# Kernel tuning notes

Hardware: AMD Instinct MI355X
Metric: run time of the kernel (lower is better)

## Reference

```python
import jax, jax.numpy as jnp
import numpy as np
from jax import lax

BN_EPS = 1e-5


def conv(x, w, b, pad):
    # x: NCHW, w: OIHW
    y = lax.conv_general_dilated(x, w, (1, 1), [(pad, pad), (pad, pad)],
                                 dimension_numbers=('NCHW', 'OIHW', 'NCHW'))
    return y + b[None, :, None, None]


def conv_t(x, w, b):
    # ConvTranspose2d, stride=1, padding=0, kernel 3. w is torch layout [in, out, kh, kw].
    # Equivalent to a regular conv with spatially flipped kernel, in/out swapped, full padding (kh-1=2).
    wf = jnp.transpose(jnp.flip(w, (2, 3)), (1, 0, 2, 3))  # [out, in, kh, kw]
    y = lax.conv_general_dilated(x, wf, (1, 1), [(2, 2), (2, 2)],
                                 dimension_numbers=('NCHW', 'OIHW', 'NCHW'))
    return y + b[None, :, None, None]


def bn(x, g, be):
    # BatchNorm2d, training-mode batch stats (biased variance), gamma/beta learnable.
    mu = x.mean((0, 2, 3), keepdims=True)
    var = x.var((0, 2, 3), keepdims=True)
    xn = (x - mu) * lax.rsqrt(var + BN_EPS)
    return g[None, :, None, None] * xn + be[None, :, None, None]


def setup_inputs() -> dict:
    key = jax.random.key(0)
    ks = jax.random.split(key, 20)
    B, C, H, W = 16, 64, 44, 44
    P = H * W  # 1936

    def kaiming(k, shape, fan_out):
        return jax.random.normal(k, shape, jnp.float32) * np.sqrt(2.0 / fan_out)

    inp = {
        'depth': jax.random.normal(ks[0], (B, C, H, W), jnp.float32),
        'rgb': jax.random.normal(ks[1], (B, C, H, W), jnp.float32),
        # h_c / h_f conv layers: Conv2d(128, 64, 3, padding=1)
        'w_hc': kaiming(ks[2], (64, 128, 3, 3), 64 * 9), 'b_hc': jnp.zeros((64,), jnp.float32),
        'w_hf': kaiming(ks[3], (64, 128, 3, 3), 64 * 9), 'b_hf': jnp.zeros((64,), jnp.float32),
        # spatial_pool_agr
        'w_s1': kaiming(ks[4], (32, P, 3, 3), 32 * 9), 'bs1': jnp.zeros((32,), jnp.float32),
        'g1': jnp.ones((32,), jnp.float32), 'be1': jnp.zeros((32,), jnp.float32),
        'w_s2': kaiming(ks[5], (32, 32, 3, 3), 32 * 9), 'bs2': jnp.zeros((32,), jnp.float32),
        'g2': jnp.ones((32,), jnp.float32), 'be2': jnp.zeros((32,), jnp.float32),
        # ConvTranspose2d weights in torch layout [in, out, kh, kw]
        'w_d1': kaiming(ks[6], (32, 32, 3, 3), 32 * 9), 'bd1': jnp.zeros((32,), jnp.float32),
        'g3': jnp.ones((32,), jnp.float32), 'be3': jnp.zeros((32,), jnp.float32),
        'w_d2': kaiming(ks[7], (32, 1, 3, 3), 1 * 9), 'bd2': jnp.zeros((1,), jnp.float32),
        # channel_pool_ag: Linear(64, 16), Linear(16, 64)
        'w_l1': kaiming(ks[8], (16, 64), 16), 'bl1': jnp.zeros((16,), jnp.float32),
        'w_l2': kaiming(ks[9], (64, 16), 64), 'bl2': jnp.zeros((64,), jnp.float32),
    }
    return inp


def reference(depth, rgb, w_hc, b_hc, w_hf, b_hf,
              w_s1, bs1, g1, be1, w_s2, bs2, g2, be2,
              w_d1, bd1, g3, be3, w_d2, bd2,
              w_l1, bl1, w_l2, bl2):
    B, C, H, W = depth.shape
    # fused rgb+depth conv
    h_c = jnp.concatenate([rgb, depth], axis=1)          # [B, 2C, H, W]
    h_c_conv = jax.nn.relu(conv(h_c, w_hc, b_hc, 1))      # [B, 64, H, W]

    # per-pixel correlation: grouped 1x1 conv == batched matmul
    # pixel_corr[b, p, y, x] = sum_c rgb[b, c, y, x] * depth[b, c, p]
    pixel_corr = jnp.einsum('bchw,bcp->bphw', rgb, depth.reshape(B, C, H * W))

    x = jax.nn.relu(bn(conv(pixel_corr, w_s1, bs1, 0), g1, be1))  # 44 -> 42
    x = jax.nn.relu(bn(conv(x, w_s2, bs2, 0), g2, be2))           # 42 -> 40
    x = jax.nn.relu(bn(conv_t(x, w_d1, bd1), g3, be3))            # 40 -> 42
    spatial_att = jax.nn.sigmoid(conv_t(x, w_d2, bd2))            # [B, 1, 44, 44]

    # per-channel correlation: grouped full-extent conv == elementwise dot per (b, c)
    depth_corr = jnp.sum(rgb * depth, axis=(2, 3))                # [B, C]
    # MaxPool2d(1)/AvgPool2d(1) are identities -> both branches are identical
    def mlp(v):
        return jax.nn.relu(v @ w_l1.T + bl1) @ w_l2.T + bl2
    m = mlp(depth_corr)
    channel_att = jax.nn.sigmoid(m + m)[:, :, None, None]         # [B, C, 1, 1]

    h_att = jnp.concatenate([h_c_conv * spatial_att, h_c_conv * channel_att], axis=1)
    return jax.nn.relu(conv(h_att, w_hf, b_hf, 1))                # [B, 64, 44, 44]
```

## Files before the change

kernel.cpp:

```cpp
#include <hip/hip_runtime.h>
#include <math.h>

#define P_ 1936
#define EPS_ 1e-5f

typedef __attribute__((ext_vector_type(8))) short bf16x8;
typedef __attribute__((ext_vector_type(4))) float f32x4;
typedef __attribute__((ext_vector_type(4))) ushort u16x4;

__device__ __forceinline__ ushort f2bf(float f) {
    union { float f; unsigned u; } v; v.f = f;
    unsigned u = v.u;
    return (ushort)((u + 0x7FFFu + ((u >> 16) & 1u)) >> 16);
}
__device__ __forceinline__ float bf2f(ushort h) {
    union { unsigned u; float f; } v; v.u = (unsigned)h << 16;
    return v.f;
}

__device__ __forceinline__ void bn_coef(const float* stats, const float* g,
                                        const float* be, int ch, float inv_n,
                                        float& sc, float& sh) {
    float sum = stats[ch*2], sq = stats[ch*2+1];
    float mu = sum * inv_n;
    float var = sq * inv_n - mu*mu;
    float r = rsqrtf(var + EPS_);
    sc = g[ch] * r;
    sh = be[ch] - mu * sc;
}

__global__ __launch_bounds__(256) void k_setup(const float* __restrict__ whc,
                                               const float* __restrict__ whf,
                                               const float* __restrict__ ws2,
                                               const float* __restrict__ wd1,
                                               const float* __restrict__ ws1,
                                               const float* __restrict__ rgb,
                                               const float* __restrict__ depth,
                                               ushort* __restrict__ wpck,
                                               ushort* __restrict__ a2,
                                               ushort* __restrict__ a3,
                                               ushort* __restrict__ apck1,
                                               ushort* __restrict__ xp,
                                               ushort* __restrict__ depthb,
                                               float* __restrict__ dcor_part,
                                               float* __restrict__ stats) {
    __shared__ float r8[8];
    const int bx = blockIdx.x, t = threadIdx.x;
    if (bx < 2808) {
        if (bx == 0 && t < 192) stats[t] = 0.f;
        int idx = bx * 256 + t;
        if (idx < 147456) {
            const float* src = (idx < 73728) ? whc : whf;
            int j = (idx < 73728) ? idx : idx - 73728;
            int kk = j / 8192, rem = j - kk * 8192;
            int o = rem >> 7, c = rem & 127;
            wpck[(idx < 73728 ? 0 : 73728) + (kk * 64 + o) * 128 + c] =
                f2bf(src[(size_t)(o * 128 + c) * 9 + kk]);
        } else if (idx < 156672) {
            int j = idx - 147456;
            int kk = j >> 10, rem = j & 1023, o = rem >> 5, c = rem & 31;
            a2[j] = f2bf(ws2[((size_t)o*32 + c)*9 + kk]);
            a3[j] = f2bf(wd1[((size_t)c*32 + o)*9 + (8 - kk)]);
        } else if (idx < 718848) {
            int j = idx - 156672;
            int m = j / 1952, p = j - m*1952;
            int o = m / 9, kk = m - o*9;
            apck1[j] = (p < P_) ? f2bf(ws1[((size_t)o*P_ + p)*9 + kk]) : (ushort)0;
        }
        return;
    }
    const int j = bx - 2808;
    const int g8 = j & 7, b = (j >> 3) & 15, q = j >> 7;
    const int c0 = g8 * 8;
    const float* rsrc = rgb   + ((size_t)b*64 + c0)*P_;
    const float* dsrc = depth + ((size_t)b*64 + c0)*P_;
    ushort* xr = xp + ((size_t)(b*16 + g8))*2300*8;
    ushort* xd = xp + ((size_t)(b*16 + 8 + g8))*2300*8;
    if (t < 8) r8[t] = 0.f;
    __syncthreads();
    float dc[8];
    #pragma unroll
    for (int e = 0; e < 8; ++e) dc[e] = 0.f;

    const int pbase = q * 575;
    for (int pos = pbase + t; pos < pbase + 575; pos += 256) {
        int y1 = pos / 50, x1 = pos - y1*50;
        uint4 vr = {0u,0u,0u,0u}, vd = {0u,0u,0u,0u};
        if (y1 >= 1 && y1 <= 44 && x1 >= 1 && x1 <= 44) {
            int p = (y1-1)*44 + (x1-1);
            ushort hr[8], hd[8];
            #pragma unroll
            for (int e = 0; e < 8; ++e) {
                float fr = rsrc[(size_t)e*P_ + p];
                float fd = dsrc[(size_t)e*P_ + p];
                dc[e] = fmaf(fr, fd, dc[e]);
                hr[e] = f2bf(fr); hd[e] = f2bf(fd);
            }
            vr.x = hr[0] | ((unsigned)hr[1] << 16); vr.y = hr[2] | ((unsigned)hr[3] << 16);
            vr.z = hr[4] | ((unsigned)hr[5] << 16); vr.w = hr[6] | ((unsigned)hr[7] << 16);
            vd.x = hd[0] | ((unsigned)hd[1] << 16); vd.y = hd[2] | ((unsigned)hd[3] << 16);
            vd.z = hd[4] | ((unsigned)hd[5] << 16); vd.w = hd[6] | ((unsigned)hd[7] << 16);
        }
        *(uint4*)(xr + (size_t)pos*8) = vr;
        *(uint4*)(xd + (size_t)pos*8) = vd;
    }
    for (int idx = q*976 + t; idx < q*976 + 976; idx += 256) {
        int e = idx / 488, jj = idx - e*488;
        u16x4 h = {0,0,0,0};
        if (jj < 484) {
            float4 f4 = *(const float4*)(dsrc + (size_t)e*P_ + jj*4);
            h[0] = f2bf(f4.x); h[1] = f2bf(f4.y); h[2] = f2bf(f4.z); h[3] = f2bf(f4.w);
        }
        *(u16x4*)(depthb + ((size_t)(b*64 + c0 + e))*1952 + jj*4) = h;
    }
    #pragma unroll
    for (int e = 0; e < 8; ++e) {
        float v = dc[e];
        #pragma unroll
        for (int off = 32; off > 0; off >>= 1) v += __shfl_down(v, off, 64);
        if ((t & 63) == 0) atomicAdd(&r8[e], v);
    }
    __syncthreads();
    if (t < 8) dcor_part[q*1024 + b*64 + c0 + t] = r8[t];
}

__global__ __launch_bounds__(256) void k_front(const ushort* __restrict__ xp,
                                               const ushort* __restrict__ wt,
                                               const float* __restrict__ bhc,
                                               ushort* __restrict__ hcp,
                                               const ushort* __restrict__ apck1,
                                               const ushort* __restrict__ depthb,
                                               ushort* __restrict__ upck,
                                               const float* __restrict__ dcor_part,
                                               const float* __restrict__ wl1,
                                               const float* __restrict__ bl1,
                                               const float* __restrict__ wl2,
                                               const float* __restrict__ bl2,
                                               float* __restrict__ catt) {
    __shared__ ushort lds[9616];
    __shared__ float mlpb[80];
    const int bx = blockIdx.x, t = threadIdx.x;
    if (bx < 352) {
        const int rt = bx % 11, og = (bx / 11) & 1, b = bx / 22;
        const int w = t >> 6, lane = t & 63, lr = lane & 15, lg = lane >> 4;
        const int r0 = rt * 4;
        f32x4 acc[2][3];
        #pragma unroll
        for (int mf = 0; mf < 2; ++mf)
            #pragma unroll
            for (int nf = 0; nf < 3; ++nf)
                acc[mf][nf] = (f32x4){0.f, 0.f, 0.f, 0.f};

        for (int s = 0; s < 4; ++s) {
            __syncthreads();
            const ushort* gsrc = xp + ((size_t)(b*16 + s*4))*2300*8;
            for (int u = t; u < 1200; u += 256) {
                int cg = u / 300, rem = u - cg*300;
                int rr = rem / 50, xx = rem - rr*50;
                uint4 v = *(const uint4*)(gsrc + (((size_t)cg*46 + (r0+rr))*50 + xx)*8);
                *(uint4*)(lds + (size_t)u*8) = v;
            }
            __syncthreads();
            const int abase = s*32 + lg*8;
            #pragma unroll
            for (int kk = 0; kk < 9; ++kk) {
                bf16x8 af[2];
                #pragma unroll
                for (int mf = 0; mf < 2; ++mf)
                    af[mf] = *(const bf16x8*)(wt + (size_t)(kk*64 + og*32 + mf*16 + lr)*128 + abase);
                const int ky = kk / 3, kx = kk - ky*3;
                #pragma unroll
                for (int nf = 0; nf < 3; ++nf) {
                    bf16x8 bf = *(const bf16x8*)&lds[((lg*6 + (w + ky))*50 + (nf*16 + lr + kx))*8];
                    #pragma unroll
                    for (int mf = 0; mf < 2; ++mf)
                        acc[mf][nf] = __builtin_amdgcn_mfma_f32_16x16x32_bf16(af[mf], bf, acc[mf][nf], 0, 0, 0);
                }
            }
        }
        const int y = r0 + w;
        #pragma unroll
        for (int nf = 0; nf < 3; ++nf) {
            int x = nf*16 + lr;
            if (x < 44) {
                #pragma unroll
                for (int mf = 0; mf < 2; ++mf) {
                    u16x4 pk;
                    #pragma unroll
                    for (int i = 0; i < 4; ++i) {
                        int ol = og*32 + mf*16 + lg*4 + i;
                        pk[i] = f2bf(fmaxf(acc[mf][nf][i] + bhc[ol], 0.f));
                    }
                    int g = og*4 + mf*2 + (lg >> 1);
                    *(u16x4*)(hcp + (((size_t)(b*8 + g)*46 + (y+1))*50 + (x+1))*8 + (lg&1)*4) = pk;
                }
            }
        }
        return;
    }
    const int j = bx - 352;
    const int mt = j % 19, b = j / 19;
    if (mt == 18) {
        float* dcs = mlpb;
        float* h   = mlpb + 64;
        if (t < 64) dcs[t] = dcor_part[b*64 + t] + dcor_part[1024 + b*64 + t]
                           + dcor_part[2048 + b*64 + t] + dcor_part[3072 + b*64 + t];
        __syncthreads();
        if (t < 16) {
            float a = bl1[t];
            #pragma unroll 8
            for (int c = 0; c < 64; ++c) a = fmaf(dcs[c], wl1[t*64 + c], a);
            h[t] = fmaxf(a, 0.f);
        }
        __syncthreads();
        if (t < 64) {
            float m = bl2[t];
            #pragma unroll
            for (int jj = 0; jj < 16; ++jj) m = fmaf(h[jj], wl2[t*16 + jj], m);
            catt[b*64 + t] = 1.f / (1.f + expf(-2.f*m));
        }
        return;
    }
    const int nt = t >> 6, lane = t & 63, lr = lane & 15, lg = lane >> 4;
    f32x4 acc = (f32x4){0.f, 0.f, 0.f, 0.f};
    const ushort* ap = apck1 + (size_t)(mt*16 + lr)*1952 + lg*8;
    const ushort* bp = depthb + ((size_t)(b*64) + nt*16 + lr)*1952 + lg*8;
    #pragma unroll 4
    for (int ks = 0; ks < 61; ++ks) {
        bf16x8 af = *(const bf16x8*)(ap + ks*32);
        bf16x8 bf = *(const bf16x8*)(bp + ks*32);
        acc = __builtin_amdgcn_mfma_f32_16x16x32_bf16(af, bf, acc, 0, 0, 0);
    }
    #pragma unroll
    for (int i = 0; i < 4; ++i) {
        int m = mt*16 + lg*4 + i;
        int o = m / 9, kk = m - o*9;
        upck[((size_t)(b*9 + kk)*32 + o)*64 + nt*16 + lr] = f2bf(acc[i]);
    }
}

__global__ __launch_bounds__(256) void k_conv1_mfma(const ushort* __restrict__ xp,
                                                    const ushort* __restrict__ upck,
                                                    const float* __restrict__ bs1,
                                                    ushort* __restrict__ z1p,
                                                    float* __restrict__ stats) {
    __shared__ ushort lds[8*6*50*8 + 32];
    __shared__ float ssum[32], ssq[32];
    const int rt = blockIdx.x, b = blockIdx.y, t = threadIdx.x;
    const int w = t >> 6, lane = t & 63, lr = lane & 15, lg = lane >> 4;
    const int r0 = rt * 4;
    if (t < 32) { ssum[t] = 0.f; ssq[t] = 0.f; }
    f32x4 acc[2][3];
    #pragma unroll
    for (int mf = 0; mf < 2; ++mf)
        #pragma unroll
        for (int nf = 0; nf < 3; ++nf)
            acc[mf][nf] = (f32x4){0.f, 0.f, 0.f, 0.f};

    const ushort* gsrc = xp + (size_t)b*16*2300*8;
    for (int u = t; u < 2400; u += 256) {
        int cg = u / 300, rem = u - cg*300;
        int rr = rem / 50, xx = rem - rr*50;
        int y1 = min(r0 + 1 + rr, 45);
        *(uint4*)(lds + (size_t)u*8) = *(const uint4*)(gsrc + (((size_t)cg*46 + y1)*50 + xx)*8);
    }
    __syncthreads();
    #pragma unroll
    for (int s = 0; s < 2; ++s) {
        #pragma unroll
        for (int kk = 0; kk < 9; ++kk) {
            bf16x8 af[2];
            #pragma unroll
            for (int mf = 0; mf < 2; ++mf)
                af[mf] = *(const bf16x8*)(upck + ((size_t)(b*9 + kk)*32 + mf*16 + lr)*64 + s*32 + lg*8);
            const int ky = kk / 3, kx = kk - ky*3;
            #pragma unroll
            for (int nf = 0; nf < 3; ++nf) {
                bf16x8 bv = *(const bf16x8*)&lds[(((s*4 + lg)*6 + (w + ky))*50 + (nf*16 + lr + kx + 1))*8];
                #pragma unroll
                for (int mf = 0; mf < 2; ++mf)
                    acc[mf][nf] = __builtin_amdgcn_mfma_f32_16x16x32_bf16(af[mf], bv, acc[mf][nf], 0, 0, 0);
            }
        }
    }
    const int y = r0 + w;
    const int cb = lg*4;
    if (y < 42) {
        float ls[2][4], lq[2][4], br[2][4];
        #pragma unroll
        for (int mf = 0; mf < 2; ++mf)
            #pragma unroll
            for (int i = 0; i < 4; ++i) {
                ls[mf][i] = 0.f; lq[mf][i] = 0.f;
                br[mf][i] = bs1[mf*16 + cb + i];
            }
        #pragma unroll
        for (int nf = 0; nf < 3; ++nf) {
            int x = nf*16 + lr;
            bool xv = (x < 42);
            #pragma unroll
            for (int mf = 0; mf < 2; ++mf) {
                u16x4 pk;
                #pragma unroll
                for (int i = 0; i < 4; ++i) {
                    float v = acc[mf][nf][i] + br[mf][i];
                    if (xv) { ls[mf][i] += v; lq[mf][i] = fmaf(v, v, lq[mf][i]); }
                    pk[i] = f2bf(v);
                }
                if (xv) {
                    int cg1 = mf*2 + (lg >> 1);
                    *(u16x4*)(z1p + ((((size_t)b*4 + cg1)*42 + y)*48 + x)*8 + (lg&1)*4) = pk;
                }
            }
        }
        #pragma unroll
        for (int mf = 0; mf < 2; ++mf)
            #pragma unroll
            for (int i = 0; i < 4; ++i) {
                float s0 = ls[mf][i], q0 = lq[mf][i];
                #pragma unroll
                for (int m = 1; m < 16; m <<= 1) { s0 += __shfl_xor(s0, m, 64); q0 += __shfl_xor(q0, m, 64); }
                if (lr == 0) { atomicAdd(&ssum[mf*16 + cb + i], s0); atomicAdd(&ssq[mf*16 + cb + i], q0); }
            }
    }
    __syncthreads();
    if (t < 32) { atomicAdd(&stats[t*2], ssum[t]); atomicAdd(&stats[t*2+1], ssq[t]); }
}

__global__ __launch_bounds__(256) void k_conv2_mfma(const ushort* __restrict__ z1p,
                                                    const ushort* __restrict__ apck,
                                                    const float* __restrict__ bs2,
                                                    const float* __restrict__ g1,
                                                    const float* __restrict__ be1,
                                                    const float* __restrict__ statsIn,
                                                    ushort* __restrict__ z2p,
                                                    float* __restrict__ statsOut) {
    __shared__ ushort lds[4*6*48*8 + 32];
    __shared__ float sc[32], sh[32], ssum[32], ssq[32];
    const int rt = blockIdx.x, b = blockIdx.y, t = threadIdx.x;
    const int w = t >> 6, lane = t & 63, lr = lane & 15, lg = lane >> 4;
    const int r0 = rt * 4;
    if (t < 32) {
        bn_coef(statsIn, g1, be1, t, 1.f/28224.f, sc[t], sh[t]);
        ssum[t] = 0.f; ssq[t] = 0.f;
    }
    __syncthreads();
    f32x4 acc[2][3];
    #pragma unroll
    for (int mf = 0; mf < 2; ++mf)
        #pragma unroll
        for (int nf = 0; nf < 3; ++nf)
            acc[mf][nf] = (f32x4){0.f, 0.f, 0.f, 0.f};

    for (int u = t; u < 1152; u += 256) {
        int cg = u / 288, rem = u - cg*288;
        int rr = rem / 48, xx = rem - rr*48;
        uint4 raw = *(const uint4*)(z1p + ((((size_t)b*4 + cg)*42 + (r0 + rr))*48 + xx)*8);
        unsigned arr[4] = {raw.x, raw.y, raw.z, raw.w};
        ushort h[8];
        #pragma unroll
        for (int e = 0; e < 8; ++e) {
            ushort hv = (e & 1) ? (ushort)(arr[e>>1] >> 16) : (ushort)(arr[e>>1] & 0xffffu);
            float f = fmaxf(fmaf(bf2f(hv), sc[cg*8 + e], sh[cg*8 + e]), 0.f);
            h[e] = f2bf(f);
        }
        uint4 v;
        v.x = h[0] | ((unsigned)h[1] << 16);
        v.y = h[2] | ((unsigned)h[3] << 16);
        v.z = h[4] | ((unsigned)h[5] << 16);
        v.w = h[6] | ((unsigned)h[7] << 16);
        *(uint4*)(lds + (size_t)u*8) = v;
    }
    __syncthreads();
    #pragma unroll
    for (int kk = 0; kk < 9; ++kk) {
        bf16x8 af[2];
        #pragma unroll
        for (int mf = 0; mf < 2; ++mf)
            af[mf] = *(const bf16x8*)(apck + (size_t)(kk*32 + mf*16 + lr)*32 + lg*8);
        const int ky = kk / 3, kx = kk - ky*3;
        #pragma unroll
        for (int nf = 0; nf < 3; ++nf) {
            bf16x8 bv = *(const bf16x8*)&lds[((lg*6 + (w + ky))*48 + (nf*16 + lr + kx))*8];
            #pragma unroll
            for (int mf = 0; mf < 2; ++mf)
                acc[mf][nf] = __builtin_amdgcn_mfma_f32_16x16x32_bf16(af[mf], bv, acc[mf][nf], 0, 0, 0);
        }
    }
    const int y = r0 + w;
    const int cb = lg*4;
    {
        float ls[2][4], lq[2][4], br[2][4];
        #pragma unroll
        for (int mf = 0; mf < 2; ++mf)
            #pragma unroll
            for (int i = 0; i < 4; ++i) {
                ls[mf][i] = 0.f; lq[mf][i] = 0.f;
                br[mf][i] = bs2[mf*16 + cb + i];
            }
        #pragma unroll
        for (int nf = 0; nf < 3; ++nf) {
            int x = nf*16 + lr;
            bool xv = (x < 40);
            #pragma unroll
            for (int mf = 0; mf < 2; ++mf) {
                u16x4 pk;
                #pragma unroll
                for (int i = 0; i < 4; ++i) {
                    float v = acc[mf][nf][i] + br[mf][i];
                    if (xv) { ls[mf][i] += v; lq[mf][i] = fmaf(v, v, lq[mf][i]); }
                    pk[i] = f2bf(v);
                }
                if (xv) {
                    int cg1 = mf*2 + (lg >> 1);
                    *(u16x4*)(z2p + ((((size_t)b*4 + cg1)*46 + (y+2))*48 + (x+2))*8 + (lg&1)*4) = pk;
                }
            }
        }
        #pragma unroll
        for (int mf = 0; mf < 2; ++mf)
            #pragma unroll
            for (int i = 0; i < 4; ++i) {
                float s0 = ls[mf][i], q0 = lq[mf][i];
                #pragma unroll
                for (int m = 1; m < 16; m <<= 1) { s0 += __shfl_xor(s0, m, 64); q0 += __shfl_xor(q0, m, 64); }
                if (lr == 0) { atomicAdd(&ssum[mf*16 + cb + i], s0); atomicAdd(&ssq[mf*16 + cb + i], q0); }
            }
    }
    __syncthreads();
    if (t < 32) { atomicAdd(&statsOut[t*2], ssum[t]); atomicAdd(&statsOut[t*2+1], ssq[t]); }
}

__global__ __launch_bounds__(256) void k_dconv1_mfma(const ushort* __restrict__ z2p,
                                                     const ushort* __restrict__ apck,
                                                     const float* __restrict__ bd1,
                                                     const float* __restrict__ g2,
                                                     const float* __restrict__ be2,
                                                     const float* __restrict__ statsIn,
                                                     ushort* __restrict__ z3p,
                                                     float* __restrict__ statsOut) {
    __shared__ ushort lds[4*6*48*8 + 32];
    __shared__ float sc[32], sh[32], ssum[32], ssq[32];
    const int rt = blockIdx.x, b = blockIdx.y, t = threadIdx.x;
    const int w = t >> 6, lane = t & 63, lr = lane & 15, lg = lane >> 4;
    const int r0 = rt * 4;
    if (t < 32) {
        bn_coef(statsIn, g2, be2, t, 1.f/25600.f, sc[t], sh[t]);
        ssum[t] = 0.f; ssq[t] = 0.f;
    }
    __syncthreads();
    f32x4 acc[2][3];
    #pragma unroll
    for (int mf = 0; mf < 2; ++mf)
        #pragma unroll
        for (int nf = 0; nf < 3; ++nf)
            acc[mf][nf] = (f32x4){0.f, 0.f, 0.f, 0.f};

    for (int u = t; u < 1152; u += 256) {
        int cg = u / 288, rem = u - cg*288;
        int rr = rem / 48, xx = rem - rr*48;
        int row = r0 + rr;
        uint4 v = {0u,0u,0u,0u};
        if (row >= 2 && row <= 41 && xx >= 2 && xx <= 41) {
            uint4 raw = *(const uint4*)(z2p + ((((size_t)b*4 + cg)*46 + row)*48 + xx)*8);
            unsigned arr[4] = {raw.x, raw.y, raw.z, raw.w};
            ushort h[8];
            #pragma unroll
            for (int e = 0; e < 8; ++e) {
                ushort hv = (e & 1) ? (ushort)(arr[e>>1] >> 16) : (ushort)(arr[e>>1] & 0xffffu);
                float f = fmaxf(fmaf(bf2f(hv), sc[cg*8 + e], sh[cg*8 + e]), 0.f);
                h[e] = f2bf(f);
            }
            v.x = h[0] | ((unsigned)h[1] << 16);
            v.y = h[2] | ((unsigned)h[3] << 16);
            v.z = h[4] | ((unsigned)h[5] << 16);
            v.w = h[6] | ((unsigned)h[7] << 16);
        }
        *(uint4*)(lds + (size_t)u*8) = v;
    }
    __syncthreads();
    #pragma unroll
    for (int kk = 0; kk < 9; ++kk) {
        bf16x8 af[2];
        #pragma unroll
        for (int mf = 0; mf < 2; ++mf)
            af[mf] = *(const bf16x8*)(apck + (size_t)(kk*32 + mf*16 + lr)*32 + lg*8);
        const int ky = kk / 3, kx = kk - ky*3;
        #pragma unroll
        for (int nf = 0; nf < 3; ++nf) {
            bf16x8 bv = *(const bf16x8*)&lds[((lg*6 + (w + ky))*48 + (nf*16 + lr + kx))*8];
            #pragma unroll
            for (int mf = 0; mf < 2; ++mf)
                acc[mf][nf] = __builtin_amdgcn_mfma_f32_16x16x32_bf16(af[mf], bv, acc[mf][nf], 0, 0, 0);
        }
    }
    const int y = r0 + w;
    const int cb = lg*4;
    if (y < 42) {
        float ls[2][4], lq[2][4], br[2][4];
        #pragma unroll
        for (int mf = 0; mf < 2; ++mf)
            #pragma unroll
            for (int i = 0; i < 4; ++i) {
                ls[mf][i] = 0.f; lq[mf][i] = 0.f;
                br[mf][i] = bd1[mf*16 + cb + i];
            }
        #pragma unroll
        for (int nf = 0; nf < 3; ++nf) {
            int x = nf*16 + lr;
            bool xv = (x < 42);
            #pragma unroll
            for (int mf = 0; mf < 2; ++mf) {
                u16x4 pk;
                #pragma unroll
                for (int i = 0; i < 4; ++i) {
                    float v = acc[mf][nf][i] + br[mf][i];
                    if (xv) { ls[mf][i] += v; lq[mf][i] = fmaf(v, v, lq[mf][i]); }
                    pk[i] = f2bf(v);
                }
                if (xv) {
                    int cg1 = mf*2 + (lg >> 1);
                    *(u16x4*)(z3p + ((((size_t)b*4 + cg1)*46 + (y+2))*48 + (x+2))*8 + (lg&1)*4) = pk;
                }
            }
        }
        #pragma unroll
        for (int mf = 0; mf < 2; ++mf)
            #pragma unroll
            for (int i = 0; i < 4; ++i) {
                float s0 = ls[mf][i], q0 = lq[mf][i];
                #pragma unroll
                for (int m = 1; m < 16; m <<= 1) { s0 += __shfl_xor(s0, m, 64); q0 += __shfl_xor(q0, m, 64); }
                if (lr == 0) { atomicAdd(&ssum[mf*16 + cb + i], s0); atomicAdd(&ssq[mf*16 + cb + i], q0); }
            }
    }
    __syncthreads();
    if (t < 32) { atomicAdd(&statsOut[t*2], ssum[t]); atomicAdd(&statsOut[t*2+1], ssq[t]); }
}

__global__ __launch_bounds__(256) void k_dconv2(const ushort* __restrict__ z3p,
                                                const float* __restrict__ wd2,
                                                const float* __restrict__ bd2,
                                                const float* __restrict__ g3,
                                                const float* __restrict__ be3,
                                                const float* __restrict__ stats,
                                                float* __restrict__ satt) {
    __shared__ float sc[32], sh[32], wf[32][9];
    const int b = blockIdx.y, t = threadIdx.x;
    if (t < 32) bn_coef(stats, g3, be3, t, 1.f/28224.f, sc[t], sh[t]);
    for (int u = t; u < 288; u += 256) {
        int c = u / 9, k = u - c*9;
        wf[c][k] = wd2[c*9 + 8 - k];
    }
    __syncthreads();
    const int pix = blockIdx.x * 256 + t;
    if (pix >= P_) return;
    const int y = pix / 44, x = pix - y*44;
    float acc = bd2[0];
    #pragma unroll
    for (int kk = 0; kk < 9; ++kk) {
        int ky = kk / 3, kx = kk - ky*3;
        int ry = y + ky, rx = x + kx;
        if (ry < 2 || ry > 43 || rx < 2 || rx > 43) continue;
        #pragma unroll
        for (int cg = 0; cg < 4; ++cg) {
            uint4 raw = *(const uint4*)(z3p + ((((size_t)b*4 + cg)*46 + ry)*48 + rx)*8);
            unsigned arr[4] = {raw.x, raw.y, raw.z, raw.w};
            #pragma unroll
            for (int e = 0; e < 8; ++e) {
                ushort hv = (e & 1) ? (ushort)(arr[e>>1] >> 16) : (ushort)(arr[e>>1] & 0xffffu);
                float f = fmaxf(fmaf(bf2f(hv), sc[cg*8 + e], sh[cg*8 + e]), 0.f);
                acc = fmaf(f, wf[cg*8 + e][kk], acc);
            }
        }
    }
    satt[(size_t)b*P_ + pix] = 1.f / (1.f + expf(-acc));
}

__global__ __launch_bounds__(256) void k_final(const ushort* __restrict__ hcp,
                                               const float* __restrict__ satt,
                                               const float* __restrict__ catt,
                                               const ushort* __restrict__ wt,
                                               const float* __restrict__ bias,
                                               float* __restrict__ out) {
    __shared__ ushort lds[9616];
    __shared__ float catv[64];
    const int rt = blockIdx.x, og = blockIdx.y, b = blockIdx.z, t = threadIdx.x;
    const int w = t >> 6, lane = t & 63, lr = lane & 15, lg = lane >> 4;
    const int r0 = rt * 4;
    if (t < 64) catv[t] = catt[b*64 + t];
    f32x4 acc[2][3];
    #pragma unroll
    for (int mf = 0; mf < 2; ++mf)
        #pragma unroll
        for (int nf = 0; nf < 3; ++nf)
            acc[mf][nf] = (f32x4){0.f, 0.f, 0.f, 0.f};

    for (int s = 0; s < 4; ++s) {
        __syncthreads();
        for (int u = t; u < 1200; u += 256) {
            int cg = u / 300, rem = u - cg*300;
            int rr = rem / 50, xx = rem - rr*50;
            int g = s*4 + cg;
            int y1 = r0 + rr;
            uint4 v = {0u,0u,0u,0u};
            if (y1 >= 1 && y1 <= 44 && xx >= 1 && xx <= 44) {
                int gs = (g < 8) ? g : (g - 8);
                uint4 raw = *(const uint4*)(hcp + (((size_t)(b*8 + gs)*46 + y1)*50 + xx)*8);
                unsigned arr[4] = {raw.x, raw.y, raw.z, raw.w};
                ushort h[8];
                if (g < 8) {
                    float att = satt[(size_t)b*P_ + (y1-1)*44 + (xx-1)];
                    #pragma unroll
                    for (int e = 0; e < 8; ++e) {
                        ushort hv = (e & 1) ? (ushort)(arr[e>>1] >> 16) : (ushort)(arr[e>>1] & 0xffffu);
                        h[e] = f2bf(bf2f(hv) * att);
                    }
                } else {
                    #pragma unroll
                    for (int e = 0; e < 8; ++e) {
                        ushort hv = (e & 1) ? (ushort)(arr[e>>1] >> 16) : (ushort)(arr[e>>1] & 0xffffu);
                        h[e] = f2bf(bf2f(hv) * catv[(g-8)*8 + e]);
                    }
                }
                v.x = h[0] | ((unsigned)h[1] << 16);
                v.y = h[2] | ((unsigned)h[3] << 16);
                v.z = h[4] | ((unsigned)h[5] << 16);
                v.w = h[6] | ((unsigned)h[7] << 16);
            }
            *(uint4*)(lds + (size_t)u*8) = v;
        }
        __syncthreads();
        const int abase = s*32 + lg*8;
        #pragma unroll
        for (int kk = 0; kk < 9; ++kk) {
            bf16x8 af[2];
            #pragma unroll
            for (int mf = 0; mf < 2; ++mf)
                af[mf] = *(const bf16x8*)(wt + (size_t)(kk*64 + og*32 + mf*16 + lr)*128 + abase);
            const int ky = kk / 3, kx = kk - ky*3;
            #pragma unroll
            for (int nf = 0; nf < 3; ++nf) {
                bf16x8 bf = *(const bf16x8*)&lds[((lg*6 + (w + ky))*50 + (nf*16 + lr + kx))*8];
                #pragma unroll
                for (int mf = 0; mf < 2; ++mf)
                    acc[mf][nf] = __builtin_amdgcn_mfma_f32_16x16x32_bf16(af[mf], bf, acc[mf][nf], 0, 0, 0);
            }
        }
    }
    const int y = r0 + w;
    #pragma unroll
    for (int nf = 0; nf < 3; ++nf) {
        int x = nf*16 + lr;
        if (x < 44) {
            #pragma unroll
            for (int mf = 0; mf < 2; ++mf) {
                #pragma unroll
                for (int i = 0; i < 4; ++i) {
                    int o = og*32 + mf*16 + lg*4 + i;
                    out[(((size_t)b*64 + o)*44 + y)*44 + x] = fmaxf(acc[mf][nf][i] + bias[o], 0.f);
                }
            }
        }
    }
}

extern "C" void kernel_launch(void* const* d_in, const int* in_sizes, int n_in,
                              void* d_out, int out_size, void* d_ws, size_t ws_size,
                              hipStream_t stream) {
    const float* depth = (const float*)d_in[0];
    const float* rgb   = (const float*)d_in[1];
    const float* w_hc  = (const float*)d_in[2];
    const float* b_hc  = (const float*)d_in[3];
    const float* w_hf  = (const float*)d_in[4];
    const float* b_hf  = (const float*)d_in[5];
    const float* w_s1  = (const float*)d_in[6];
    const float* bs1   = (const float*)d_in[7];
    const float* g1    = (const float*)d_in[8];
    const float* be1   = (const float*)d_in[9];
    const float* w_s2  = (const float*)d_in[10];
    const float* bs2   = (const float*)d_in[11];
    const float* g2    = (const float*)d_in[12];
    const float* be2   = (const float*)d_in[13];
    const float* w_d1  = (const float*)d_in[14];
    const float* bd1   = (const float*)d_in[15];
    const float* g3    = (const float*)d_in[16];
    const float* be3   = (const float*)d_in[17];
    const float* w_d2  = (const float*)d_in[18];
    const float* bd2   = (const float*)d_in[19];
    const float* w_l1  = (const float*)d_in[20];
    const float* bl1   = (const float*)d_in[21];
    const float* w_l2  = (const float*)d_in[22];
    const float* bl2   = (const float*)d_in[23];

    float* out = (float*)d_out;
    float* ws  = (float*)d_ws;

    float*    satt   = ws;
    float*    catt   = satt + 30976;
    float*    dcorp  = catt + 1024;
    float*    stats  = dcorp + 4096;
    ushort* hcp    = (ushort*)(stats + 192);
    ushort* wpck   = hcp    + 2355200;
    ushort* apck2  = wpck   + 147456;
    ushort* apck3  = apck2  + 9216;
    ushort* apck1  = apck3  + 9216;
    ushort* depthb = apck1  + 562176;
    ushort* upck   = depthb + 1998848;
    ushort* z1p    = upck   + 294912;
    ushort* z2p    = z1p    + 1032192;
    ushort* z3p    = z2p    + 1130496;
    ushort* xpck   = z3p    + 1130496;

    k_setup<<<3320, 256, 0, stream>>>(w_hc, w_hf, w_s2, w_d1, w_s1, rgb, depth,
                                      wpck, apck2, apck3, apck1, xpck, depthb,
                                      dcorp, stats);

    k_front<<<656, 256, 0, stream>>>(xpck, wpck, b_hc, hcp,
                                     apck1, depthb, upck,
                                     dcorp, w_l1, bl1, w_l2, bl2, catt);

    k_conv1_mfma<<<dim3(11,16), 256, 0, stream>>>(xpck, upck, bs1, z1p, stats);
    k_conv2_mfma<<<dim3(10,16), 256, 0, stream>>>(z1p, apck2, bs2, g1, be1, stats, z2p, stats + 64);
    k_dconv1_mfma<<<dim3(11,16), 256, 0, stream>>>(z2p, apck3, bd1, g2, be2, stats + 64, z3p, stats + 128);
    k_dconv2<<<dim3(8,16), 256, 0, stream>>>(z3p, w_d2, bd2, g3, be3, stats + 128, satt);

    k_final<<<dim3(11,2,16), 256, 0, stream>>>(hcp, satt, catt, wpck + 73728, b_hf, out);
}
```

Before: 136.2 us.

## Fuse spatial-attention deconv into final conv kernel with halo recompute

Removes the separate k_dconv2 launch and computes the sigmoid spatial attention for each block's 4-row tile plus a one-row halo directly inside k_final, keeping it in shared memory. This eliminates one kernel launch and the global round-trip of the attention map. In exchange, each attention row is recomputed by several blocks (both output-channel groups and overlapping halos), and the extra prologue lengthens k_final.

New measurement: 174.9 us. 1.28x slower.

```diff
diff --git a/kernel.cpp b/kernel.cpp
--- a/kernel.cpp
+++ b/kernel.cpp
@@ -538,57 +538,56 @@
     if (t < 32) { atomicAdd(&statsOut[t*2], ssum[t]); atomicAdd(&statsOut[t*2+1], ssq[t]); }
 }
 
-__global__ __launch_bounds__(256) void k_dconv2(const ushort* __restrict__ z3p,
-                                                const float* __restrict__ wd2,
-                                                const float* __restrict__ bd2,
-                                                const float* __restrict__ g3,
-                                                const float* __restrict__ be3,
-                                                const float* __restrict__ stats,
-                                                float* __restrict__ satt) {
-    __shared__ float sc[32], sh[32], wf[32][9];
-    const int b = blockIdx.y, t = threadIdx.x;
-    if (t < 32) bn_coef(stats, g3, be3, t, 1.f/28224.f, sc[t], sh[t]);
-    for (int u = t; u < 288; u += 256) {
-        int c = u / 9, k = u - c*9;
-        wf[c][k] = wd2[c*9 + 8 - k];
-    }
-    __syncthreads();
-    const int pix = blockIdx.x * 256 + t;
-    if (pix >= P_) return;
-    const int y = pix / 44, x = pix - y*44;
-    float acc = bd2[0];
-    #pragma unroll
-    for (int kk = 0; kk < 9; ++kk) {
-        int ky = kk / 3, kx = kk - ky*3;
-        int ry = y + ky, rx = x + kx;
-        if (ry < 2 || ry > 43 || rx < 2 || rx > 43) continue;
-        #pragma unroll
-        for (int cg = 0; cg < 4; ++cg) {
-            uint4 raw = *(const uint4*)(z3p + ((((size_t)b*4 + cg)*46 + ry)*48 + rx)*8);
-            unsigned arr[4] = {raw.x, raw.y, raw.z, raw.w};
-            #pragma unroll
-            for (int e = 0; e < 8; ++e) {
-                ushort hv = (e & 1) ? (ushort)(arr[e>>1] >> 16) : (ushort)(arr[e>>1] & 0xffffu);
-                float f = fmaxf(fmaf(bf2f(hv), sc[cg*8 + e], sh[cg*8 + e]), 0.f);
-                acc = fmaf(f, wf[cg*8 + e][kk], acc);
-            }
-        }
-    }
-    satt[(size_t)b*P_ + pix] = 1.f / (1.f + expf(-acc));
-}
-
 __global__ __launch_bounds__(256) void k_final(const ushort* __restrict__ hcp,
-                                               const float* __restrict__ satt,
+                                               const ushort* __restrict__ z3p,
+                                               const float* __restrict__ wd2,
+                                               const float* __restrict__ bd2,
+                                               const float* __restrict__ g3,
+                                               const float* __restrict__ be3,
+                                               const float* __restrict__ stats3,
                                                const float* __restrict__ catt,
                                                const ushort* __restrict__ wt,
                                                const float* __restrict__ bias,
                                                float* __restrict__ out) {
     __shared__ ushort lds[9616];
     __shared__ float catv[64];
+    __shared__ float satt_s[264];
+    __shared__ float scv[32], shv[32], wfv[288];
     const int rt = blockIdx.x, og = blockIdx.y, b = blockIdx.z, t = threadIdx.x;
     const int w = t >> 6, lane = t & 63, lr = lane & 15, lg = lane >> 4;
     const int r0 = rt * 4;
     if (t < 64) catv[t] = catt[b*64 + t];
+    if (t >= 64 && t < 96) bn_coef(stats3, g3, be3, t - 64, 1.f/28224.f, scv[t-64], shv[t-64]);
+    for (int u = t; u < 288; u += 256) {
+        int c = u / 9, k = u - c*9;
+        wfv[c*9 + k] = wd2[c*9 + 8 - k];
+    }
+    __syncthreads();
+    for (int u = t; u < 264; u += 256) {
+        int syi = u / 44, x = u - syi*44;
+        int sy = r0 - 1 + syi;
+        if (sy >= 0 && sy < 44) {
+            float acc = bd2[0];
+            #pragma unroll
+            for (int kk = 0; kk < 9; ++kk) {
+                int ky = kk / 3, kx = kk - ky*3;
+                int ry = sy + ky, rx = x + kx;
+                if (ry < 2 || ry > 43 || rx < 2 || rx > 43) continue;
+                #pragma unroll
+                for (int cg = 0; cg < 4; ++cg) {
+                    uint4 raw = *(const uint4*)(z3p + ((((size_t)b*4 + cg)*46 + ry)*48 + rx)*8);
+                    unsigned arr[4] = {raw.x, raw.y, raw.z, raw.w};
+                    #pragma unroll
+                    for (int e = 0; e < 8; ++e) {
+                        ushort hv = (e & 1) ? (ushort)(arr[e>>1] >> 16) : (ushort)(arr[e>>1] & 0xffffu);
+                        float f = fmaxf(fmaf(bf2f(hv), scv[cg*8 + e], shv[cg*8 + e]), 0.f);
+                        acc = fmaf(f, wfv[(cg*8 + e)*9 + kk], acc);
+                    }
+                }
+            }
+            satt_s[u] = 1.f / (1.f + expf(-acc));
+        }
+    }
     f32x4 acc[2][3];
     #pragma unroll
     for (int mf = 0; mf < 2; ++mf)
@@ -610,7 +609,7 @@
                 unsigned arr[4] = {raw.x, raw.y, raw.z, raw.w};
                 ushort h[8];
                 if (g < 8) {
-                    float att = satt[(size_t)b*P_ + (y1-1)*44 + (xx-1)];
+                    float att = satt_s[(y1 - r0)*44 + (xx - 1)];
                     #pragma unroll
                     for (int e = 0; e < 8; ++e) {
                         ushort hv = (e & 1) ? (ushort)(arr[e>>1] >> 16) : (ushort)(arr[e>>1] & 0xffffu);
@@ -696,8 +695,7 @@
     float* out = (float*)d_out;
     float* ws  = (float*)d_ws;
 
-    float*    satt   = ws;
-    float*    catt   = satt + 30976;
+    float*    catt   = ws;
     float*    dcorp  = catt + 1024;
     float*    stats  = dcorp + 4096;
     ushort* hcp    = (ushort*)(stats + 192);
@@ -723,7 +721,7 @@
     k_conv1_mfma<<<dim3(11,16), 256, 0, stream>>>(xpck, upck, bs1, z1p, stats);
     k_conv2_mfma<<<dim3(10,16), 256, 0, stream>>>(z1p, apck2, bs2, g1, be1, stats, z2p, stats + 64);
     k_dconv1_mfma<<<dim3(11,16), 256, 0, stream>>>(z2p, apck3, bd1, g2, be2, stats + 64, z3p, stats + 128);
-    k_dconv2<<<dim3(8,16), 256, 0, stream>>>(z3p, w_d2, bd2, g3, be3, stats + 128, satt);
-
-    k_final<<<dim3(11,2,16), 256, 0, stream>>>(hcp, satt, catt, wpck + 73728, b_hf, out);
-}
+
+    k_final<<<dim3(11,2,16), 256, 0, stream>>>(hcp, z3p, w_d2, bd2, g3, be3, stats + 128,
+                                               catt, wpck + 73728, b_hf, out);
+}
```
